# Performance work log

Hardware: AMD Instinct MI355X
Metric: run time of the kernel (lower is better)

Reference implementation:

```python
import jax, jax.numpy as jnp
import numpy as np
import math

B, S, D, H = 2, 2048, 1024, 16
DH = D // H  # dim_per_head = 64


def setup_inputs() -> dict:
    key = jax.random.key(0)
    ks = jax.random.split(key, 12)
    s = 1.0 / math.sqrt(D)
    return {
        "key": jax.random.normal(ks[0], (B, S, D), jnp.float32),
        "value": jax.random.normal(ks[1], (B, S, D), jnp.float32),
        "query": jax.random.normal(ks[2], (B, S, D), jnp.float32),
        "mask": jax.random.randint(ks[3], (B, S, S), 0, 2).astype(bool),
        "Wq": jax.random.normal(ks[4], (D, D), jnp.float32) * s,
        "bq": jnp.zeros((D,), jnp.float32),
        "Wk": jax.random.normal(ks[5], (D, D), jnp.float32) * s,
        "bk": jnp.zeros((D,), jnp.float32),
        "Wv": jax.random.normal(ks[6], (D, D), jnp.float32) * s,
        "bv": jnp.zeros((D,), jnp.float32),
        "Wo": jax.random.normal(ks[7], (D, D), jnp.float32) * s,
        "bo": jnp.zeros((D,), jnp.float32),
    }


def _shape(x):
    # [B, S, D] -> [B, H, S, DH]
    return x.reshape(B, -1, H, DH).transpose(0, 2, 1, 3)


def reference(key, value, query, mask, Wq, bq, Wk, bk, Wv, bv, Wo, bo):
    q = _shape(query @ Wq.T + bq)  # [B,H,Sq,DH]
    k = _shape(key @ Wk.T + bk)    # [B,H,Sk,DH]
    v = _shape(value @ Wv.T + bv)  # [B,H,Sk,DH]
    q = q / jnp.sqrt(jnp.asarray(DH, q.dtype))
    scores = jnp.einsum("bhqd,bhkd->bhqk", q, k)
    scores = jnp.where(mask[:, None, :, :], jnp.asarray(-1e18, scores.dtype), scores)
    attn = jax.nn.softmax(scores, axis=-1)
    # dropout is identity in eval/deterministic reference
    ctx = jnp.einsum("bhqk,bhkd->bhqd", attn, v)
    ctx = ctx.transpose(0, 2, 1, 3).reshape(B, -1, D)  # unshape
    return ctx @ Wo.T + bo
```

## Files before the change

kernel.cpp:

```cpp
#include <hip/hip_runtime.h>
#include <math.h>


constexpr int Bc  = 2;
constexpr int Sc  = 2048;
constexpr int Dc  = 1024;
constexpr int Hc  = 16;
constexpr int DHc = 64;
constexpr int BSc = Bc * Sc;

constexpr float LOG2E = 1.4426950408889634f;

typedef __bf16 bf16x8 __attribute__((ext_vector_type(8)));
typedef __bf16 bf16x4 __attribute__((ext_vector_type(4)));
typedef float  f32x4  __attribute__((ext_vector_type(4)));

#define GLDS16(gp, lp) __builtin_amdgcn_global_load_lds( \
    (const __attribute__((address_space(1))) void*)(gp), \
    (__attribute__((address_space(3))) void*)(lp), 16, 0, 0)

__global__ __launch_bounds__(256)
void wsplit(const float* __restrict__ W0, const float* __restrict__ W1,
            const float* __restrict__ W2, const float* __restrict__ W3,
            __bf16* __restrict__ out)
{
    const float* src[4] = {W0, W1, W2, W3};
    const int z = blockIdx.y;
    const size_t idx = ((size_t)blockIdx.x * 256 + threadIdx.x) * 4;
    const float4 v = *(const float4*)&src[z][idx];
    bf16x4 o;
    o[0] = (__bf16)v.x; o[1] = (__bf16)v.y; o[2] = (__bf16)v.z; o[3] = (__bf16)v.w;
    *(bf16x4*)&out[(size_t)z * Dc * Dc + idx] = o;
}

__device__ __forceinline__ void sweep128s(const float* __restrict__ A,
                                          const __bf16* __restrict__ Wh,
                                          __bf16* As, __bf16* Ws,
                                          int gm0, int gn0, f32x4 acc[4][4])
{
    const int tid  = threadIdx.x;
    const int w    = tid >> 6;
    const int lane = tid & 63;
    const int cc   = lane & 15;
    const int g    = lane >> 4;
    const int wm   = (w & 1) * 64;
    const int wn   = (w >> 1) * 64;

    for (int k0 = 0; k0 < Dc; k0 += 64) {
        __syncthreads();
#pragma unroll
        for (int r = 0; r < 4; ++r) {
            const int L  = r * 256 + tid;
            const int wr = L >> 3;
            const int sl = L & 7;
            const int c  = sl ^ (wr & 7);
            GLDS16(Wh + (size_t)(gn0 + wr) * Dc + k0 + c * 8,
                   (char*)Ws + (r * 256 + w * 64) * 16);
        }
#pragma unroll
        for (int i = 0; i < 8; ++i) {
            const int Lq = i * 256 + tid;
            const int ar = Lq >> 4;
            const int aq = Lq & 15;
            const float4 v = *(const float4*)&A[(size_t)(gm0 + ar) * Dc + k0 + aq * 4];
            const int off = ar * 128 +
                        ((((aq >> 1) ^ (ar & 7)) << 4) | ((aq & 1) << 3));
            bf16x4 hv;
            hv[0] = (__bf16)v.x; hv[1] = (__bf16)v.y;
            hv[2] = (__bf16)v.z; hv[3] = (__bf16)v.w;
            *(bf16x4*)((char*)As + off) = hv;
        }
        __syncthreads();
#pragma unroll
        for (int kk = 0; kk < 2; ++kk) {
            const int cb4 = (kk * 4 + g) << 4;
            bf16x8 af[4], bfr[4];
#pragma unroll
            for (int mt = 0; mt < 4; ++mt) {
                const int row = wm + mt * 16 + cc;
                af[mt] = *(const bf16x8*)((const char*)As + row * 128 +
                                          (cb4 ^ ((row & 7) << 4)));
            }
#pragma unroll
            for (int nt = 0; nt < 4; ++nt) {
                const int row = wn + nt * 16 + cc;
                bfr[nt] = *(const bf16x8*)((const char*)Ws + row * 128 +
                                           (cb4 ^ ((row & 7) << 4)));
            }
#pragma unroll
            for (int mt = 0; mt < 4; ++mt)
#pragma unroll
                for (int nt = 0; nt < 4; ++nt)
                    acc[mt][nt] = __builtin_amdgcn_mfma_f32_16x16x32_bf16(
                        af[mt], bfr[nt], acc[mt][nt], 0, 0, 0);
        }
    }
}

__device__ __forceinline__ void sweep64b(const __bf16* __restrict__ Ahi,
                                         const __bf16* __restrict__ Alo,
                                         const __bf16* __restrict__ Wh,
                                         __bf16* AsHi, __bf16* AsLo, __bf16* Ws,
                                         int gm0, int gn0, f32x4 acc[2][4])
{
    const int tid  = threadIdx.x;
    const int w    = tid >> 6;
    const int lane = tid & 63;
    const int cc   = lane & 15;
    const int g    = lane >> 4;
    const int wm   = (w & 1) * 32;
    const int wn   = (w >> 1) * 64;

    for (int k0 = 0; k0 < Dc; k0 += 64) {
        __syncthreads();
#pragma unroll
        for (int r = 0; r < 4; ++r) {
            const int L  = r * 256 + tid;
            const int wr = L >> 3;
            const int sl = L & 7;
            const int c  = sl ^ (wr & 7);
            GLDS16(Wh + (size_t)(gn0 + wr) * Dc + k0 + c * 8,
                   (char*)Ws + (r * 256 + w * 64) * 16);
        }
#pragma unroll
        for (int r = 0; r < 2; ++r) {
            const int L  = r * 256 + tid;
            const int wr = L >> 3;
            const int sl = L & 7;
            const int c  = sl ^ (wr & 7);
            GLDS16(Ahi + (size_t)(gm0 + wr) * Dc + k0 + c * 8,
                   (char*)AsHi + (r * 256 + w * 64) * 16);
            GLDS16(Alo + (size_t)(gm0 + wr) * Dc + k0 + c * 8,
                   (char*)AsLo + (r * 256 + w * 64) * 16);
        }
        __syncthreads();
#pragma unroll
        for (int kk = 0; kk < 2; ++kk) {
            const int cb4 = (kk * 4 + g) << 4;
            bf16x8 ahi[2], alo[2], bfr[4];
#pragma unroll
            for (int mt = 0; mt < 2; ++mt) {
                const int row = wm + mt * 16 + cc;
                const int off = row * 128 + (cb4 ^ ((row & 7) << 4));
                ahi[mt] = *(const bf16x8*)((const char*)AsHi + off);
                alo[mt] = *(const bf16x8*)((const char*)AsLo + off);
            }
#pragma unroll
            for (int nt = 0; nt < 4; ++nt) {
                const int row = wn + nt * 16 + cc;
                bfr[nt] = *(const bf16x8*)((const char*)Ws + row * 128 +
                                           (cb4 ^ ((row & 7) << 4)));
            }
#pragma unroll
            for (int mt = 0; mt < 2; ++mt)
#pragma unroll
                for (int nt = 0; nt < 4; ++nt) {
                    acc[mt][nt] = __builtin_amdgcn_mfma_f32_16x16x32_bf16(
                        ahi[mt], bfr[nt], acc[mt][nt], 0, 0, 0);
                    acc[mt][nt] = __builtin_amdgcn_mfma_f32_16x16x32_bf16(
                        alo[mt], bfr[nt], acc[mt][nt], 0, 0, 0);
                }
        }
    }
}

__global__ __launch_bounds__(256)
void qkv_mfma(const float* __restrict__ query, const float* __restrict__ key,
              const float* __restrict__ value, const __bf16* __restrict__ Whi,
              const float* __restrict__ bq, const float* __restrict__ bk,
              const float* __restrict__ bv,
              __bf16* __restrict__ Qo, __bf16* __restrict__ Ko, __bf16* __restrict__ Vt)
{
    __shared__ __align__(16) __bf16 As[8192];
    __shared__ __align__(16) __bf16 Ws[8192];

    const int z = blockIdx.z;
    const float* A    = (z == 0) ? query : (z == 1) ? key : value;
    const float* bias = (z == 0) ? bq    : (z == 1) ? bk  : bv;
    const float scale = (z == 0) ? 0.125f * LOG2E : 1.0f;
    const __bf16* Wh  = Whi + (size_t)z * Dc * Dc;

    const int gm0 = blockIdx.x * 128;
    const int gn0 = blockIdx.y * 128;

    f32x4 acc[4][4];
#pragma unroll
    for (int mt = 0; mt < 4; ++mt)
#pragma unroll
        for (int nt = 0; nt < 4; ++nt) acc[mt][nt] = {0.f, 0.f, 0.f, 0.f};

    sweep128s(A, Wh, As, Ws, gm0, gn0, acc);

    const int tid = threadIdx.x;
    const int w = tid >> 6, lane = tid & 63;
    const int cc = lane & 15, g = lane >> 4;
    const int wm = (w & 1) * 64, wn = (w >> 1) * 64;

    float bias4[4];
#pragma unroll
    for (int nt = 0; nt < 4; ++nt) bias4[nt] = bias[gn0 + wn + nt * 16 + cc];

    if (z == 2) {
#pragma unroll
        for (int mt = 0; mt < 4; ++mt)
#pragma unroll
            for (int nt = 0; nt < 4; ++nt) {
                const int col = gn0 + wn + nt * 16 + cc;
                const int h = col >> 6, dh = col & 63;
                const int row0 = gm0 + wm + mt * 16 + g * 4;
                const int b = row0 >> 11, s0 = row0 & 2047;
                bf16x4 vv;
#pragma unroll
                for (int reg = 0; reg < 4; ++reg)
                    vv[reg] = (__bf16)(acc[mt][nt][reg] + bias4[nt]);
                *(bf16x4*)&Vt[(((size_t)(b * Hc + h)) * DHc + dh) * Sc + s0] = vv;
            }
    } else {
        __bf16* O = (z == 0) ? Qo : Ko;
#pragma unroll
        for (int mt = 0; mt < 4; ++mt)
#pragma unroll
            for (int nt = 0; nt < 4; ++nt) {
                const int col = gn0 + wn + nt * 16 + cc;
                const int h = col >> 6, dh = col & 63;
#pragma unroll
                for (int reg = 0; reg < 4; ++reg) {
                    const int row = gm0 + wm + mt * 16 + g * 4 + reg;
                    const int b = row >> 11, s = row & 2047;
                    O[(((size_t)(b * Hc + h)) * Sc + s) * DHc + dh] =
                        (__bf16)((acc[mt][nt][reg] + bias4[nt]) * scale);
                }
            }
    }
}

__global__ __launch_bounds__(256)
void out_mfma(const __bf16* __restrict__ ctxHi, const __bf16* __restrict__ ctxLo,
              const __bf16* __restrict__ Wohi,
              const float* __restrict__ bo, float* __restrict__ out)
{
    __shared__ __align__(16) __bf16 AsHi[4096];
    __shared__ __align__(16) __bf16 AsLo[4096];
    __shared__ __align__(16) __bf16 Ws[8192];

    const int gm0 = blockIdx.x * 64;
    const int gn0 = blockIdx.y * 128;

    f32x4 acc[2][4];
#pragma unroll
    for (int mt = 0; mt < 2; ++mt)
#pragma unroll
        for (int nt = 0; nt < 4; ++nt) acc[mt][nt] = {0.f, 0.f, 0.f, 0.f};

    sweep64b(ctxHi, ctxLo, Wohi, AsHi, AsLo, Ws, gm0, gn0, acc);

    const int tid = threadIdx.x;
    const int w = tid >> 6, lane = tid & 63;
    const int cc = lane & 15, g = lane >> 4;
    const int wm = (w & 1) * 32, wn = (w >> 1) * 64;

    float bias4[4];
#pragma unroll
    for (int nt = 0; nt < 4; ++nt) bias4[nt] = bo[gn0 + wn + nt * 16 + cc];

#pragma unroll
    for (int mt = 0; mt < 2; ++mt)
#pragma unroll
        for (int nt = 0; nt < 4; ++nt) {
            const int col = gn0 + wn + nt * 16 + cc;
#pragma unroll
            for (int reg = 0; reg < 4; ++reg) {
                const int row = gm0 + wm + mt * 16 + g * 4 + reg;
                out[(size_t)row * Dc + col] = acc[mt][nt][reg] + bias4[nt];
            }
        }
}

__global__ __launch_bounds__(256)
void mask_pack(const int* __restrict__ mask, unsigned long long* __restrict__ out)
{
    const int lane = threadIdx.x & 63;
    const size_t waveBase = ((size_t)blockIdx.x * 4 + (threadIdx.x >> 6)) * 256;
    unsigned long long b0 = __ballot(mask[waveBase + lane]        != 0);
    unsigned long long b1 = __ballot(mask[waveBase + 64 + lane]   != 0);
    unsigned long long b2 = __ballot(mask[waveBase + 128 + lane]  != 0);
    unsigned long long b3 = __ballot(mask[waveBase + 192 + lane]  != 0);
    if (lane == 0) {
        unsigned long long* dst = out + (waveBase >> 6);
        dst[0] = b0; dst[1] = b1; dst[2] = b2; dst[3] = b3;
    }
}

__global__ __launch_bounds__(256)
void attn_mfma(const __bf16* __restrict__ Q, const __bf16* __restrict__ K,
               const __bf16* __restrict__ Vt,
               const unsigned long long* __restrict__ mp,
               __bf16* __restrict__ ctxHi, __bf16* __restrict__ ctxLo)
{
    __shared__ __bf16 Ks[64][72];
    __shared__ __bf16 Vs[64][72];
    __shared__ __align__(16) char PsB[4 * 2048];

    const int tid  = threadIdx.x;
    const int w    = tid >> 6;
    const int lane = tid & 63;
    const int cc   = lane & 15;
    const int g    = lane >> 4;
    const int bh   = blockIdx.y;
    const int b    = bh >> 4;
    const int h    = bh & 15;
    const int qw   = blockIdx.x * 64 + w * 16;

    const __bf16* Qb  = Q  + (size_t)bh * Sc * DHc;
    const __bf16* Kb  = K  + (size_t)bh * Sc * DHc;
    const __bf16* Vtb = Vt + (size_t)bh * DHc * Sc;
    char* Pw = PsB + w * 2048;

    const bf16x8 qa0 = *(const bf16x8*)&Qb[(size_t)(qw + cc) * DHc + g * 8];
    const bf16x8 qa1 = *(const bf16x8*)&Qb[(size_t)(qw + cc) * DHc + 32 + g * 8];

    f32x4 o[4] = {};
    float l[4] = {0.f, 0.f, 0.f, 0.f};

    const int str_r = tid >> 3;
    const int str_c = (tid & 7) * 8;

    bf16x8 pk0 = *(const bf16x8*)&Kb[(size_t)str_r * DHc + str_c];
    bf16x8 pk1 = *(const bf16x8*)&Kb[(size_t)(str_r + 32) * DHc + str_c];
    bf16x8 pv0 = *(const bf16x8*)&Vtb[(size_t)str_r * Sc + str_c];
    bf16x8 pv1 = *(const bf16x8*)&Vtb[(size_t)(str_r + 32) * Sc + str_c];

    for (int k0 = 0; k0 < Sc; k0 += 64) {
        __syncthreads();
        *(bf16x8*)&Ks[str_r][str_c]      = pk0;
        *(bf16x8*)&Ks[str_r + 32][str_c] = pk1;
        *(bf16x8*)&Vs[str_r][str_c]      = pv0;
        *(bf16x8*)&Vs[str_r + 32][str_c] = pv1;
        __syncthreads();

        if (k0 + 64 < Sc) {
            pk0 = *(const bf16x8*)&Kb[(size_t)(k0 + 64 + str_r) * DHc + str_c];
            pk1 = *(const bf16x8*)&Kb[(size_t)(k0 + 64 + str_r + 32) * DHc + str_c];
            pv0 = *(const bf16x8*)&Vtb[(size_t)str_r * Sc + k0 + 64 + str_c];
            pv1 = *(const bf16x8*)&Vtb[(size_t)(str_r + 32) * Sc + k0 + 64 + str_c];
        }

        unsigned long long mw[4];
#pragma unroll
        for (int r = 0; r < 4; ++r)
            mw[r] = mp[(size_t)(b * Sc + qw + g * 4 + r) * (Sc / 64) + (k0 >> 6)];

        f32x4 sc[4];
#pragma unroll
        for (int nt = 0; nt < 4; ++nt) {
            const bf16x8 kb0 = *(const bf16x8*)&Ks[nt * 16 + cc][g * 8];
            const bf16x8 kb1 = *(const bf16x8*)&Ks[nt * 16 + cc][32 + g * 8];
            f32x4 z = {-24.f, -24.f, -24.f, -24.f};
            z = __builtin_amdgcn_mfma_f32_16x16x32_bf16(qa0, kb0, z, 0, 0, 0);
            z = __builtin_amdgcn_mfma_f32_16x16x32_bf16(qa1, kb1, z, 0, 0, 0);
            sc[nt] = z;
        }

        unsigned mlo[4], mhi[4];
#pragma unroll
        for (int r = 0; r < 4; ++r) {
            const unsigned long long sh = mw[r] >> cc;
            mlo[r] = (unsigned)sh;
            mhi[r] = (unsigned)(sh >> 32);
        }
#pragma unroll
        for (int nt = 0; nt < 4; ++nt)
#pragma unroll
            for (int r = 0; r < 4; ++r) {
                float p = __builtin_amdgcn_exp2f(sc[nt][r]);
                const unsigned bit =
                    (nt == 0) ? (mlo[r] & 1u) :
                    (nt == 1) ? (mlo[r] & 0x10000u) :
                    (nt == 2) ? (mhi[r] & 1u) : (mhi[r] & 0x10000u);
                p = bit ? 0.f : p;
                l[r] += p;
                *(__bf16*)(Pw + (g * 4 + r) * 128 + (((nt ^ g) << 5) | (cc << 1))) =
                    (__bf16)p;
            }

        const int sw = (cc >> 2) << 5;
        const bf16x8 pa0 = *(const bf16x8*)(Pw + cc * 128 + ((g * 16) ^ sw));
        const bf16x8 pa1 = *(const bf16x8*)(Pw + cc * 128 + ((64 + g * 16) ^ sw));

#pragma unroll
        for (int nt = 0; nt < 4; ++nt) {
            const bf16x8 vb0 = *(const bf16x8*)&Vs[nt * 16 + cc][g * 8];
            const bf16x8 vb1 = *(const bf16x8*)&Vs[nt * 16 + cc][32 + g * 8];
            o[nt] = __builtin_amdgcn_mfma_f32_16x16x32_bf16(pa0, vb0, o[nt], 0, 0, 0);
            o[nt] = __builtin_amdgcn_mfma_f32_16x16x32_bf16(pa1, vb1, o[nt], 0, 0, 0);
        }
    }

#pragma unroll
    for (int off = 1; off < 16; off <<= 1)
#pragma unroll
        for (int r = 0; r < 4; ++r)
            l[r] += __shfl_xor(l[r], off, 16);

#pragma unroll
    for (int r = 0; r < 4; ++r) {
        const float inv = 1.0f / l[r];
        const int q = qw + g * 4 + r;
#pragma unroll
        for (int nt = 0; nt < 4; ++nt) {
            const size_t idx = ((size_t)b * Sc + q) * Dc + h * 64 + nt * 16 + cc;
            const float v = o[nt][r] * inv;
            const __bf16 hi = (__bf16)v;
            ctxHi[idx] = hi;
            ctxLo[idx] = (__bf16)(v - (float)hi);
        }
    }
}

extern "C" void kernel_launch(void* const* d_in, const int* in_sizes, int n_in,
                              void* d_out, int out_size, void* d_ws, size_t ws_size,
                              hipStream_t stream)
{
    const float* key   = (const float*)d_in[0];
    const float* value = (const float*)d_in[1];
    const float* query = (const float*)d_in[2];
    const int*   mask  = (const int*)  d_in[3];
    const float* Wq    = (const float*)d_in[4];
    const float* bq    = (const float*)d_in[5];
    const float* Wk    = (const float*)d_in[6];
    const float* bk    = (const float*)d_in[7];
    const float* Wv    = (const float*)d_in[8];
    const float* bv    = (const float*)d_in[9];
    const float* Wo    = (const float*)d_in[10];
    const float* bo    = (const float*)d_in[11];
    float* out = (float*)d_out;

    char* wsb = (char*)d_ws;
    __bf16* Qbf  = (__bf16*)(wsb);
    __bf16* Kbf  = (__bf16*)(wsb + ((size_t)8  << 20));
    __bf16* Vt   = (__bf16*)(wsb + ((size_t)16 << 20));
    unsigned long long* mpk = (unsigned long long*)(wsb + ((size_t)32 << 20));
    __bf16* Whi  = (__bf16*)(wsb + ((size_t)33 << 20));
    __bf16* ctxHi = (__bf16*)(wsb + ((size_t)41 << 20));
    __bf16* ctxLo = (__bf16*)(wsb + ((size_t)49 << 20));

    dim3 gws(Dc * Dc / (256 * 4), 4);
    wsplit<<<gws, 256, 0, stream>>>(Wq, Wk, Wv, Wo, Whi);

    dim3 gqkv(BSc / 128, Dc / 128, 3);
    qkv_mfma<<<gqkv, 256, 0, stream>>>(query, key, value, Whi, bq, bk, bv,
                                       Qbf, Kbf, Vt);

    const int mask_n = Bc * Sc * Sc;
    mask_pack<<<mask_n / 1024, 256, 0, stream>>>(mask, mpk);

    dim3 gattn(Sc / 64, Bc * Hc);
    attn_mfma<<<gattn, 256, 0, stream>>>(Qbf, Kbf, Vt, mpk, ctxHi, ctxLo);

    dim3 gout(BSc / 64, Dc / 128);
    out_mfma<<<gout, 256, 0, stream>>>(ctxHi, ctxLo, Whi + (size_t)3 * Dc * Dc,
                                       bo, out);
}
```

Measured before the change: 295.3 us.

## Split attention key range across two wave groups per block and merge partials

The attention kernel now launches 512 threads per block. Two groups of four waves each process half of the key sequence, with separate K/V shared-memory tiles. After the loop, the second group writes its partial output and row sums to shared memory, and the first group combines them and stores the context. This doubles the waves working on each query tile to raise latency hiding and occupancy. The cost is a larger shared-memory footprint, an extra reduction step and extra block-wide syncs. The fixed softmax offset means no max rescaling is needed when merging.

```diff
diff --git a/kernel.cpp b/kernel.cpp
--- a/kernel.cpp
+++ b/kernel.cpp
@@ -291,30 +291,33 @@
     }
 }
 
-__global__ __launch_bounds__(256)
+__global__ __launch_bounds__(512, 6)
 void attn_mfma(const __bf16* __restrict__ Q, const __bf16* __restrict__ K,
                const __bf16* __restrict__ Vt,
                const unsigned long long* __restrict__ mp,
                __bf16* __restrict__ ctxHi, __bf16* __restrict__ ctxLo)
 {
-    __shared__ __bf16 Ks[64][72];
-    __shared__ __bf16 Vs[64][72];
-    __shared__ __align__(16) char PsB[4 * 2048];
+    __shared__ __align__(16) char smem[53248];
 
     const int tid  = threadIdx.x;
     const int w    = tid >> 6;
     const int lane = tid & 63;
     const int cc   = lane & 15;
     const int g    = lane >> 4;
+    const int qg   = w & 3;
+    const int kh   = w >> 2;
     const int bh   = blockIdx.y;
     const int b    = bh >> 4;
     const int h    = bh & 15;
-    const int qw   = blockIdx.x * 64 + w * 16;
+    const int qw   = blockIdx.x * 64 + qg * 16;
 
     const __bf16* Qb  = Q  + (size_t)bh * Sc * DHc;
     const __bf16* Kb  = K  + (size_t)bh * Sc * DHc;
     const __bf16* Vtb = Vt + (size_t)bh * DHc * Sc;
-    char* Pw = PsB + w * 2048;
+
+    __bf16* Ks = (__bf16*)(smem + kh * 18432);
+    __bf16* Vs = (__bf16*)(smem + kh * 18432 + 9216);
+    char*   Pw = smem + 36864 + w * 2048;
 
     const bf16x8 qa0 = *(const bf16x8*)&Qb[(size_t)(qw + cc) * DHc + g * 8];
     const bf16x8 qa1 = *(const bf16x8*)&Qb[(size_t)(qw + cc) * DHc + 32 + g * 8];
@@ -322,27 +325,31 @@
     f32x4 o[4] = {};
     float l[4] = {0.f, 0.f, 0.f, 0.f};
 
-    const int str_r = tid >> 3;
-    const int str_c = (tid & 7) * 8;
-
-    bf16x8 pk0 = *(const bf16x8*)&Kb[(size_t)str_r * DHc + str_c];
-    bf16x8 pk1 = *(const bf16x8*)&Kb[(size_t)(str_r + 32) * DHc + str_c];
-    bf16x8 pv0 = *(const bf16x8*)&Vtb[(size_t)str_r * Sc + str_c];
-    bf16x8 pv1 = *(const bf16x8*)&Vtb[(size_t)(str_r + 32) * Sc + str_c];
-
-    for (int k0 = 0; k0 < Sc; k0 += 64) {
-        __syncthreads();
-        *(bf16x8*)&Ks[str_r][str_c]      = pk0;
-        *(bf16x8*)&Ks[str_r + 32][str_c] = pk1;
-        *(bf16x8*)&Vs[str_r][str_c]      = pv0;
-        *(bf16x8*)&Vs[str_r + 32][str_c] = pv1;
-        __syncthreads();
-
-        if (k0 + 64 < Sc) {
-            pk0 = *(const bf16x8*)&Kb[(size_t)(k0 + 64 + str_r) * DHc + str_c];
-            pk1 = *(const bf16x8*)&Kb[(size_t)(k0 + 64 + str_r + 32) * DHc + str_c];
-            pv0 = *(const bf16x8*)&Vtb[(size_t)str_r * Sc + k0 + 64 + str_c];
-            pv1 = *(const bf16x8*)&Vtb[(size_t)(str_r + 32) * Sc + k0 + 64 + str_c];
+    const int t4    = tid & 255;
+    const int str_r = t4 >> 3;
+    const int str_c = (t4 & 7) * 8;
+    const int kbase = kh * (Sc / 2);
+
+    bf16x8 pk0 = *(const bf16x8*)&Kb[(size_t)(kbase + str_r) * DHc + str_c];
+    bf16x8 pk1 = *(const bf16x8*)&Kb[(size_t)(kbase + str_r + 32) * DHc + str_c];
+    bf16x8 pv0 = *(const bf16x8*)&Vtb[(size_t)str_r * Sc + kbase + str_c];
+    bf16x8 pv1 = *(const bf16x8*)&Vtb[(size_t)(str_r + 32) * Sc + kbase + str_c];
+
+    for (int it = 0; it < 16; ++it) {
+        const int k0 = kbase + it * 64;
+        __syncthreads();
+        *(bf16x8*)&Ks[(size_t)str_r * 72 + str_c]        = pk0;
+        *(bf16x8*)&Ks[(size_t)(str_r + 32) * 72 + str_c] = pk1;
+        *(bf16x8*)&Vs[(size_t)str_r * 72 + str_c]        = pv0;
+        *(bf16x8*)&Vs[(size_t)(str_r + 32) * 72 + str_c] = pv1;
+        __syncthreads();
+
+        if (it < 15) {
+            const int kn = k0 + 64;
+            pk0 = *(const bf16x8*)&Kb[(size_t)(kn + str_r) * DHc + str_c];
+            pk1 = *(const bf16x8*)&Kb[(size_t)(kn + str_r + 32) * DHc + str_c];
+            pv0 = *(const bf16x8*)&Vtb[(size_t)str_r * Sc + kn + str_c];
+            pv1 = *(const bf16x8*)&Vtb[(size_t)(str_r + 32) * Sc + kn + str_c];
         }
 
         unsigned long long mw[4];
@@ -353,8 +360,8 @@
         f32x4 sc[4];
 #pragma unroll
         for (int nt = 0; nt < 4; ++nt) {
-            const bf16x8 kb0 = *(const bf16x8*)&Ks[nt * 16 + cc][g * 8];
-            const bf16x8 kb1 = *(const bf16x8*)&Ks[nt * 16 + cc][32 + g * 8];
+            const bf16x8 kb0 = *(const bf16x8*)&Ks[(size_t)(nt * 16 + cc) * 72 + g * 8];
+            const bf16x8 kb1 = *(const bf16x8*)&Ks[(size_t)(nt * 16 + cc) * 72 + 32 + g * 8];
             f32x4 z = {-24.f, -24.f, -24.f, -24.f};
             z = __builtin_amdgcn_mfma_f32_16x16x32_bf16(qa0, kb0, z, 0, 0, 0);
             z = __builtin_amdgcn_mfma_f32_16x16x32_bf16(qa1, kb1, z, 0, 0, 0);
@@ -389,8 +396,8 @@
 
 #pragma unroll
         for (int nt = 0; nt < 4; ++nt) {
-            const bf16x8 vb0 = *(const bf16x8*)&Vs[nt * 16 + cc][g * 8];
-            const bf16x8 vb1 = *(const bf16x8*)&Vs[nt * 16 + cc][32 + g * 8];
+            const bf16x8 vb0 = *(const bf16x8*)&Vs[(size_t)(nt * 16 + cc) * 72 + g * 8];
+            const bf16x8 vb1 = *(const bf16x8*)&Vs[(size_t)(nt * 16 + cc) * 72 + 32 + g * 8];
             o[nt] = __builtin_amdgcn_mfma_f32_16x16x32_bf16(pa0, vb0, o[nt], 0, 0, 0);
             o[nt] = __builtin_amdgcn_mfma_f32_16x16x32_bf16(pa1, vb1, o[nt], 0, 0, 0);
         }
@@ -402,17 +409,35 @@
         for (int r = 0; r < 4; ++r)
             l[r] += __shfl_xor(l[r], off, 16);
 
-#pragma unroll
-    for (int r = 0; r < 4; ++r) {
-        const float inv = 1.0f / l[r];
-        const int q = qw + g * 4 + r;
-#pragma unroll
-        for (int nt = 0; nt < 4; ++nt) {
-            const size_t idx = ((size_t)b * Sc + q) * Dc + h * 64 + nt * 16 + cc;
-            const float v = o[nt][r] * inv;
-            const __bf16 hi = (__bf16)v;
-            ctxHi[idx] = hi;
-            ctxLo[idx] = (__bf16)(v - (float)hi);
+    __syncthreads();
+    float* Oc = (float*)smem;
+    float* Lc = (float*)(smem + 16384);
+    if (kh) {
+#pragma unroll
+        for (int nt = 0; nt < 4; ++nt)
+#pragma unroll
+            for (int r = 0; r < 4; ++r)
+                Oc[(qg * 16 + g * 4 + r) * 64 + nt * 16 + cc] = o[nt][r];
+        if (cc == 0)
+#pragma unroll
+            for (int r = 0; r < 4; ++r) Lc[qg * 16 + g * 4 + r] = l[r];
+    }
+    __syncthreads();
+    if (!kh) {
+#pragma unroll
+        for (int r = 0; r < 4; ++r) {
+            const float lt = l[r] + Lc[qg * 16 + g * 4 + r];
+            const float inv = 1.0f / lt;
+            const int q = qw + g * 4 + r;
+#pragma unroll
+            for (int nt = 0; nt < 4; ++nt) {
+                const size_t idx = ((size_t)b * Sc + q) * Dc + h * 64 + nt * 16 + cc;
+                const float v =
+                    (o[nt][r] + Oc[(qg * 16 + g * 4 + r) * 64 + nt * 16 + cc]) * inv;
+                const __bf16 hi = (__bf16)v;
+                ctxHi[idx] = hi;
+                ctxLo[idx] = (__bf16)(v - (float)hi);
+            }
         }
     }
 }
@@ -455,7 +480,7 @@
     mask_pack<<<mask_n / 1024, 256, 0, stream>>>(mask, mpk);
 
     dim3 gattn(Sc / 64, Bc * Hc);
-    attn_mfma<<<gattn, 256, 0, stream>>>(Qbf, Kbf, Vt, mpk, ctxHi, ctxLo);
+    attn_mfma<<<gattn, 512, 0, stream>>>(Qbf, Kbf, Vt, mpk, ctxHi, ctxLo);
 
     dim3 gout(BSc / 64, Dc / 128);
     out_mfma<<<gout, 256, 0, stream>>>(ctxHi, ctxLo, Whi + (size_t)3 * Dc * Dc,
```

Result: no change. 300.1 us (+1.6%).
